# Performance work log

Measured on AMD Instinct MI355X. Metric: run time of the kernel, lower is better.

Reference implementation:

```python
import jax, jax.numpy as jnp
import numpy as np

EPS_NORM = 1e-12   # F.normalize eps
EPS_SCALE = 1e-5   # activation scale clamp


def _weight_quant(w):
    # ternary (sign) quantization with mean-abs scale
    scale = jnp.mean(jnp.abs(w))
    u = jnp.sign(w - jnp.mean(w))
    return u, scale


def _activation_quant(x):
    # SimpleRMSNorm: l2-normalize over last dim, times dim**-0.5
    dim_scale = x.shape[-1] ** -0.5
    l2 = jnp.linalg.norm(x, axis=-1, keepdims=True)
    xn = x / jnp.maximum(l2, EPS_NORM) * dim_scale
    # per-token int8 scale
    scale = 127.0 / jnp.maximum(jnp.max(jnp.abs(xn), axis=-1, keepdims=True), EPS_SCALE)
    y = jnp.clip(jnp.round(xn * scale), -128.0, 127.0)
    return y, scale


def setup_inputs() -> dict:
    key = jax.random.key(0)
    kx, kw, kb = jax.random.split(key, 3)
    B, S, D, O = 4, 8192, 1024, 1024
    x = jax.random.normal(kx, (B, S, D), dtype=jnp.float32)
    w = jax.random.normal(kw, (O, D), dtype=jnp.float32)
    b = jax.random.normal(kb, (O,), dtype=jnp.float32)
    return {"x": x, "w": w, "b": b}


def reference(x, w, b):
    w_q, w_scale = _weight_quant(w)          # [O,D], scalar
    b_q, b_scale = _weight_quant(b)          # [O], scalar
    x_q, x_scale = _activation_quant(x)      # [B,S,D], [B,S,1]
    # mm + broadcast bias add, then dequant by product of all three scales
    y = jnp.einsum('bsd,od->bso', x_q, w_q) + b_q
    return y / (w_scale * x_scale * b_scale)
```

## Files before the change

### kernel.cpp

```cpp
#include <hip/hip_runtime.h>
#include <cstdint>
#include <cstddef>


typedef __attribute__((ext_vector_type(4))) int int4v;

static constexpr int DIM = 1024;
static constexpr int OUTF = 1024;
static constexpr int MROWS = 32768;
static constexpr float INV_WN = 1.0f / (1024.0f * 1024.0f);
static constexpr float INV_BN = 1.0f / 1024.0f;

#define OFF_XSCALE 1024
#define OFF_WQ 132096
#define OFF_XQ 1180672

__device__ inline float wave_sum(float v) {
#pragma unroll
  for (int off = 32; off; off >>= 1) v += __shfl_xor(v, off);
  return v;
}
__device__ inline float wave_max(float v) {
#pragma unroll
  for (int off = 32; off; off >>= 1) v = fmaxf(v, __shfl_xor(v, off));
  return v;
}

__global__ __launch_bounds__(256) void reduce_wb(const float* __restrict__ w,
                                                 const float* __restrict__ b,
                                                 float* __restrict__ red) {
  __shared__ float ss[4], sa[4];
  const int t = threadIdx.x;
  const int lane = t & 63, wv = t >> 6;
  float s = 0.0f, a = 0.0f;
  const float4* w4 = (const float4*)w;
  const int idx = blockIdx.x * 256 + t;
#pragma unroll
  for (int i = 0; i < 4; ++i) {
    float4 v = w4[idx + i * 65536];
    s += (v.x + v.y) + (v.z + v.w);
    a += (fabsf(v.x) + fabsf(v.y)) + (fabsf(v.z) + fabsf(v.w));
  }
  s = wave_sum(s);
  a = wave_sum(a);
  if (lane == 0) { ss[wv] = s; sa[wv] = a; }
  __syncthreads();
  if (t == 0) atomicAdd(&red[0], (ss[0] + ss[1]) + (ss[2] + ss[3]));
  if (t == 1) atomicAdd(&red[1], (sa[0] + sa[1]) + (sa[2] + sa[3]));
  if (blockIdx.x == 0) {
    __syncthreads();
    float4 v = ((const float4*)b)[t];
    float s2 = (v.x + v.y) + (v.z + v.w);
    float a2 = (fabsf(v.x) + fabsf(v.y)) + (fabsf(v.z) + fabsf(v.w));
    s2 = wave_sum(s2);
    a2 = wave_max(a2) * 0.0f + wave_sum(a2);
    if (lane == 0) { ss[wv] = s2; sa[wv] = a2; }
    __syncthreads();
    if (t == 0) {
      red[2] = (ss[0] + ss[1]) + (ss[2] + ss[3]);
      red[3] = (sa[0] + sa[1]) + (sa[2] + sa[3]);
    }
  }
}

__global__ __launch_bounds__(256) void quant_w(const float* __restrict__ w,
                                               const float* __restrict__ red,
                                               signed char* __restrict__ wq) {
  const float wmean = red[0] * INV_WN;
  const int idx = blockIdx.x * 256 + threadIdx.x;
  float4 v = ((const float4*)w)[idx];
  int q0, q1, q2, q3;
  float d;
  d = v.x - wmean; q0 = d > 0.f ? 1 : (d < 0.f ? -1 : 0);
  d = v.y - wmean; q1 = d > 0.f ? 1 : (d < 0.f ? -1 : 0);
  d = v.z - wmean; q2 = d > 0.f ? 1 : (d < 0.f ? -1 : 0);
  d = v.w - wmean; q3 = d > 0.f ? 1 : (d < 0.f ? -1 : 0);
  const int pk = (q0 & 0xff) | ((q1 & 0xff) << 8) | ((q2 & 0xff) << 16) | ((q3 & 0xff) << 24);
  ((int*)wq)[idx] = pk;
}

__global__ __launch_bounds__(256) void quant_x(const float* __restrict__ x,
                                               signed char* __restrict__ xq,
                                               float* __restrict__ xscale) {
  const int wv = threadIdx.x >> 6;
  const int lane = threadIdx.x & 63;
  const int row = blockIdx.x * 4 + wv;
  const float4* xr = (const float4*)(x + (size_t)row * DIM);
  float4 v[4];
  float ss = 0.0f, ma = 0.0f;
#pragma unroll
  for (int it = 0; it < 4; ++it) {
    v[it] = xr[it * 64 + lane];
    ss += v[it].x * v[it].x + v[it].y * v[it].y + v[it].z * v[it].z + v[it].w * v[it].w;
    ma = fmaxf(ma, fmaxf(fmaxf(fabsf(v[it].x), fabsf(v[it].y)),
                         fmaxf(fabsf(v[it].z), fabsf(v[it].w))));
  }
  ss = wave_sum(ss);
  ma = wave_max(ma);

  const float l2 = sqrtf(ss);
  const float inv = 0.03125f / fmaxf(l2, 1e-12f);
  const float scale = 127.0f / fmaxf(ma * inv, 1e-5f);
  const float f = inv * scale;

  int* outp = (int*)(xq + (size_t)row * DIM);
#pragma unroll
  for (int it = 0; it < 4; ++it) {
    const int q0 = (int)fminf(fmaxf(rintf(v[it].x * f), -128.f), 127.f);
    const int q1 = (int)fminf(fmaxf(rintf(v[it].y * f), -128.f), 127.f);
    const int q2 = (int)fminf(fmaxf(rintf(v[it].z * f), -128.f), 127.f);
    const int q3 = (int)fminf(fmaxf(rintf(v[it].w * f), -128.f), 127.f);
    outp[it * 64 + lane] =
        (q0 & 0xff) | ((q1 & 0xff) << 8) | ((q2 & 0xff) << 16) | ((q3 & 0xff) << 24);
  }
  if (lane == 0) xscale[row] = scale;
}

#define BM 128
#define BN 128
#define BKB 128

__global__ __launch_bounds__(256) void gemm_i8(
    const signed char* __restrict__ Aq,
    const signed char* __restrict__ Wq,
    const float* __restrict__ bias,
    const float* __restrict__ red,
    const float* __restrict__ xscale,
    float* __restrict__ out) {
  __shared__ signed char As[BM * BKB];
  __shared__ signed char Bs[BN * BKB];

  const int t = threadIdx.x;
  const int lane = t & 63;
  const int wv = t >> 6;
  const int quad = lane >> 4;
  const int r16 = lane & 15;
  const int wm = (wv >> 1) * 64;
  const int wn = (wv & 1) * 64;
  const int bm = blockIdx.y;
  const int bn = blockIdx.x;

  int4v acc[4][4] = {};

  const char* Ab = (const char*)(Aq + (size_t)bm * BM * DIM);
  const char* Bb = (const char*)(Wq + (size_t)bn * BN * DIM);

  const int srow = lane >> 3;
  const int sbyte = (lane & 7) * 16;

  for (int k0 = 0; k0 < DIM; k0 += BKB) {
#pragma unroll
    for (int i = 0; i < 4; ++i) {
      const int c = wv * 4 + i;
      const int row = c * 8 + srow;
      __builtin_amdgcn_global_load_lds(
          (const __attribute__((address_space(1))) void*)(Ab + (size_t)row * DIM + k0 + sbyte),
          (__attribute__((address_space(3))) void*)((char*)As + c * 1024 + lane * 16),
          16, 0, 0);
      __builtin_amdgcn_global_load_lds(
          (const __attribute__((address_space(1))) void*)(Bb + (size_t)row * DIM + k0 + sbyte),
          (__attribute__((address_space(3))) void*)((char*)Bs + c * 1024 + lane * 16),
          16, 0, 0);
    }
    __syncthreads();
#pragma unroll
    for (int s = 0; s < 2; ++s) {
      int4v af[4], bf[4];
#pragma unroll
      for (int i = 0; i < 4; ++i) {
        af[i] = *(const int4v*)(As + (wm + i * 16 + r16) * BKB + s * 64 + quad * 16);
        bf[i] = *(const int4v*)(Bs + (wn + i * 16 + r16) * BKB + s * 64 + quad * 16);
      }
#pragma unroll
      for (int i = 0; i < 4; ++i)
#pragma unroll
        for (int j = 0; j < 4; ++j)
          acc[i][j] = __builtin_amdgcn_mfma_i32_16x16x64_i8(af[i], bf[j], acc[i][j], 0, 0, 0);
    }
    __syncthreads();
  }

  const float wscale = red[1] * INV_WN;
  const float bscale = red[3] * INV_BN;
  const float bmean = red[2] * INV_BN;
  const float wb = wscale * bscale;

  float rec[4][4];
#pragma unroll
  for (int i = 0; i < 4; ++i)
#pragma unroll
    for (int rr = 0; rr < 4; ++rr) {
      const int m = bm * BM + wm + i * 16 + quad * 4 + rr;
      rec[i][rr] = 1.0f / (wb * xscale[m]);
    }

#pragma unroll
  for (int j = 0; j < 4; ++j) {
    const int n = bn * BN + wn + j * 16 + r16;
    const float bd = bias[n] - bmean;
    const int bq = bd > 0.f ? 1 : (bd < 0.f ? -1 : 0);
#pragma unroll
    for (int i = 0; i < 4; ++i) {
      const int mg = bm * BM + wm + i * 16 + quad * 4;
      float* po = out + (size_t)mg * OUTF + n;
#pragma unroll
      for (int rr = 0; rr < 4; ++rr)
        po[(size_t)rr * OUTF] = (float)(acc[i][j][rr] + bq) * rec[i][rr];
    }
  }
}

extern "C" void kernel_launch(void* const* d_in, const int* in_sizes, int n_in,
                              void* d_out, int out_size, void* d_ws, size_t ws_size,
                              hipStream_t stream) {
  const float* x = (const float*)d_in[0];
  const float* w = (const float*)d_in[1];
  const float* b = (const float*)d_in[2];
  float* out = (float*)d_out;
  char* ws = (char*)d_ws;

  float* red = (float*)ws;
  float* xscale = (float*)(ws + OFF_XSCALE);
  signed char* wq = (signed char*)(ws + OFF_WQ);
  signed char* xq = (signed char*)(ws + OFF_XQ);

  hipMemsetAsync(red, 0, 4 * sizeof(float), stream);
  reduce_wb<<<256, 256, 0, stream>>>(w, b, red);
  quant_w<<<1024, 256, 0, stream>>>(w, red, wq);
  quant_x<<<MROWS / 4, 256, 0, stream>>>(x, xq, xscale);
  gemm_i8<<<dim3(OUTF / BN, MROWS / BM), 256, 0, stream>>>(xq, wq, b, red, xscale, out);
}
```

Baseline: 298.2 us.

## Restructure int8 GEMM into 256x256 double-buffered tiles with swizzled LDS

The int8 GEMM moves from 128x128 tiles on 4 waves to 256x256 tiles on 8 waves. LDS is double-buffered so the next K-slice streams in through global_load_lds, with explicit vmcnt waits, while MFMAs run on the current slice. The LDS layout gets an XOR swizzle to cut bank conflicts, blocks are remapped for L2 locality, and s_setprio is raised around the MFMA bursts. A dead wave_max in the bias reduction is also removed. The cost is much higher LDS use per block (128 KB) and more accumulator registers, which limits occupancy.

```diff
diff --git a/kernel.cpp b/kernel.cpp
--- a/kernel.cpp
+++ b/kernel.cpp
@@ -53,7 +53,7 @@
     float s2 = (v.x + v.y) + (v.z + v.w);
     float a2 = (fabsf(v.x) + fabsf(v.y)) + (fabsf(v.z) + fabsf(v.w));
     s2 = wave_sum(s2);
-    a2 = wave_max(a2) * 0.0f + wave_sum(a2);
+    a2 = wave_sum(a2);
     if (lane == 0) { ss[wv] = s2; sa[wv] = a2; }
     __syncthreads();
     if (t == 0) {
@@ -116,96 +116,134 @@
   if (lane == 0) xscale[row] = scale;
 }
 
-#define BM 128
-#define BN 128
-#define BKB 128
-
-__global__ __launch_bounds__(256) void gemm_i8(
+__global__ __launch_bounds__(512, 2) void gemm_i8(
     const signed char* __restrict__ Aq,
     const signed char* __restrict__ Wq,
     const float* __restrict__ bias,
     const float* __restrict__ red,
     const float* __restrict__ xscale,
     float* __restrict__ out) {
-  __shared__ signed char As[BM * BKB];
-  __shared__ signed char Bs[BN * BKB];
+  __shared__ signed char As[2][256 * 128];
+  __shared__ signed char Bs[2][256 * 128];
 
   const int t = threadIdx.x;
   const int lane = t & 63;
   const int wv = t >> 6;
   const int quad = lane >> 4;
   const int r16 = lane & 15;
-  const int wm = (wv >> 1) * 64;
-  const int wn = (wv & 1) * 64;
-  const int bm = blockIdx.y;
-  const int bn = blockIdx.x;
-
-  int4v acc[4][4] = {};
-
-  const char* Ab = (const char*)(Aq + (size_t)bm * BM * DIM);
-  const char* Bb = (const char*)(Wq + (size_t)bn * BN * DIM);
-
-  const int srow = lane >> 3;
-  const int sbyte = (lane & 7) * 16;
-
-  for (int k0 = 0; k0 < DIM; k0 += BKB) {
-#pragma unroll
-    for (int i = 0; i < 4; ++i) {
-      const int c = wv * 4 + i;
-      const int row = c * 8 + srow;
-      __builtin_amdgcn_global_load_lds(
-          (const __attribute__((address_space(1))) void*)(Ab + (size_t)row * DIM + k0 + sbyte),
-          (__attribute__((address_space(3))) void*)((char*)As + c * 1024 + lane * 16),
-          16, 0, 0);
-      __builtin_amdgcn_global_load_lds(
-          (const __attribute__((address_space(1))) void*)(Bb + (size_t)row * DIM + k0 + sbyte),
-          (__attribute__((address_space(3))) void*)((char*)Bs + c * 1024 + lane * 16),
-          16, 0, 0);
+  const int wr = wv >> 2;
+  const int wc = wv & 3;
+
+  const int orig = blockIdx.x;
+  const int swz = (orig & 7) * 64 + (orig >> 3);
+  const int bn = swz & 3;
+  const int bm = swz >> 2;
+
+  const signed char* Ab = Aq + (size_t)bm * 256 * DIM;
+  const signed char* Bb = Wq + (size_t)bn * 256 * DIM;
+
+  const int ldsoff = lane * 16;
+  const int row8 = lane >> 3;
+  const int sw16 = (((lane & 7) ^ row8) << 4);
+
+  int4v acc[8][4] = {};
+
+#define STAGE(tt, dd)                                                            \
+  do {                                                                           \
+    const size_t koff_ = (size_t)(tt) * 128 + sw16;                              \
+    _Pragma("unroll") for (int i_ = 0; i_ < 4; ++i_) {                           \
+      const int blk_ = wv * 4 + i_;              \
+      const size_t roff_ = (size_t)(blk_ * 8 + row8) * DIM + koff_;              \
+      __builtin_amdgcn_global_load_lds(                                          \
+          (const __attribute__((address_space(1))) void*)(Ab + roff_),           \
+          (__attribute__((address_space(3))) void*)(&As[dd][blk_ * 1024 + ldsoff]), \
+          16, 0, 0);                                                             \
+      __builtin_amdgcn_global_load_lds(                                          \
+          (const __attribute__((address_space(1))) void*)(Bb + roff_),           \
+          (__attribute__((address_space(3))) void*)(&Bs[dd][blk_ * 1024 + ldsoff]), \
+          16, 0, 0);                                                             \
+    }                                                                            \
+  } while (0)
+
+#define PHASE(mq, nq, cc)                                                        \
+  do {                                                                           \
+    int4v af[4][2], bf[2][2];                                                    \
+    const int swr_ = (r16 & 7) << 4;                                             \
+    _Pragma("unroll") for (int i_ = 0; i_ < 4; ++i_) {                           \
+      const int r_ = wr * 128 + ((mq)*4 + i_) * 16 + r16;                        \
+      _Pragma("unroll") for (int s_ = 0; s_ < 2; ++s_)                           \
+          af[i_][s_] = *(const int4v*)&As[cc][r_ * 128 +                         \
+                                             ((s_ * 64 + quad * 16) ^ swr_)];    \
+    }                                                                            \
+    _Pragma("unroll") for (int j_ = 0; j_ < 2; ++j_) {                           \
+      const int r_ = wc * 64 + ((nq)*2 + j_) * 16 + r16;                         \
+      _Pragma("unroll") for (int s_ = 0; s_ < 2; ++s_)                           \
+          bf[j_][s_] = *(const int4v*)&Bs[cc][r_ * 128 +                         \
+                                             ((s_ * 64 + quad * 16) ^ swr_)];    \
+    }                                                                            \
+    asm volatile("s_barrier" ::: "memory");                                      \
+    __builtin_amdgcn_s_setprio(1);                                               \
+    _Pragma("unroll") for (int i_ = 0; i_ < 4; ++i_)                             \
+        _Pragma("unroll") for (int j_ = 0; j_ < 2; ++j_) {                       \
+      acc[(mq)*4 + i_][(nq)*2 + j_] = __builtin_amdgcn_mfma_i32_16x16x64_i8(     \
+          af[i_][0], bf[j_][0], acc[(mq)*4 + i_][(nq)*2 + j_], 0, 0, 0);         \
+      acc[(mq)*4 + i_][(nq)*2 + j_] = __builtin_amdgcn_mfma_i32_16x16x64_i8(     \
+          af[i_][1], bf[j_][1], acc[(mq)*4 + i_][(nq)*2 + j_], 0, 0, 0);         \
+    }                                                                            \
+    __builtin_amdgcn_s_setprio(0);                                               \
+    asm volatile("s_barrier" ::: "memory");                                      \
+  } while (0)
+
+#define COMPUTE(cc) \
+  PHASE(0, 0, cc);  \
+  PHASE(1, 0, cc);  \
+  PHASE(0, 1, cc);  \
+  PHASE(1, 1, cc)
+
+  STAGE(0, 0);
+#pragma unroll 1
+  for (int tp = 0; tp < 4; ++tp) {
+    STAGE(2 * tp + 1, 1);
+    asm volatile("s_waitcnt vmcnt(8)" ::: "memory");
+    asm volatile("s_barrier" ::: "memory");
+    COMPUTE(0);
+    if (tp < 3) {
+      STAGE(2 * tp + 2, 0);
+      asm volatile("s_waitcnt vmcnt(8)" ::: "memory");
+    } else {
+      asm volatile("s_waitcnt vmcnt(0)" ::: "memory");
     }
-    __syncthreads();
-#pragma unroll
-    for (int s = 0; s < 2; ++s) {
-      int4v af[4], bf[4];
-#pragma unroll
-      for (int i = 0; i < 4; ++i) {
-        af[i] = *(const int4v*)(As + (wm + i * 16 + r16) * BKB + s * 64 + quad * 16);
-        bf[i] = *(const int4v*)(Bs + (wn + i * 16 + r16) * BKB + s * 64 + quad * 16);
-      }
-#pragma unroll
-      for (int i = 0; i < 4; ++i)
-#pragma unroll
-        for (int j = 0; j < 4; ++j)
-          acc[i][j] = __builtin_amdgcn_mfma_i32_16x16x64_i8(af[i], bf[j], acc[i][j], 0, 0, 0);
-    }
-    __syncthreads();
-  }
+    asm volatile("s_barrier" ::: "memory");
+    COMPUTE(1);
+  }
+#undef COMPUTE
+#undef PHASE
+#undef STAGE
 
   const float wscale = red[1] * INV_WN;
   const float bscale = red[3] * INV_BN;
   const float bmean = red[2] * INV_BN;
   const float wb = wscale * bscale;
 
-  float rec[4][4];
-#pragma unroll
-  for (int i = 0; i < 4; ++i)
-#pragma unroll
-    for (int rr = 0; rr < 4; ++rr) {
-      const int m = bm * BM + wm + i * 16 + quad * 4 + rr;
-      rec[i][rr] = 1.0f / (wb * xscale[m]);
-    }
-
+  int bq[4];
 #pragma unroll
   for (int j = 0; j < 4; ++j) {
-    const int n = bn * BN + wn + j * 16 + r16;
-    const float bd = bias[n] - bmean;
-    const int bq = bd > 0.f ? 1 : (bd < 0.f ? -1 : 0);
-#pragma unroll
-    for (int i = 0; i < 4; ++i) {
-      const int mg = bm * BM + wm + i * 16 + quad * 4;
-      float* po = out + (size_t)mg * OUTF + n;
+    const float bd = bias[bn * 256 + wc * 64 + j * 16 + r16] - bmean;
+    bq[j] = bd > 0.f ? 1 : (bd < 0.f ? -1 : 0);
+  }
+
+#pragma unroll
+  for (int i = 0; i < 8; ++i) {
+    const int mg = bm * 256 + wr * 128 + i * 16 + quad * 4;
+    float rec[4];
+#pragma unroll
+    for (int rr = 0; rr < 4; ++rr) rec[rr] = 1.0f / (wb * xscale[mg + rr]);
+#pragma unroll
+    for (int j = 0; j < 4; ++j) {
+      float* po = out + (size_t)mg * OUTF + bn * 256 + wc * 64 + j * 16 + r16;
 #pragma unroll
       for (int rr = 0; rr < 4; ++rr)
-        po[(size_t)rr * OUTF] = (float)(acc[i][j][rr] + bq) * rec[i][rr];
+        po[(size_t)rr * OUTF] = (float)(acc[i][j][rr] + bq[j]) * rec[rr];
     }
   }
 }
@@ -228,5 +266,5 @@
   reduce_wb<<<256, 256, 0, stream>>>(w, b, red);
   quant_w<<<1024, 256, 0, stream>>>(w, red, wq);
   quant_x<<<MROWS / 4, 256, 0, stream>>>(x, xq, xscale);
-  gemm_i8<<<dim3(OUTF / BN, MROWS / BM), 256, 0, stream>>>(xq, wq, b, red, xscale, out);
-}
+  gemm_i8<<<512, 512, 0, stream>>>(xq, wq, b, red, xscale, out);
+}
```

After: 298.4 us. About the same (+0.1%).
